# Optimization experiments

Measured on AMD Instinct MI355X. Metric: run time of the kernel, lower is better.

Reference implementation:

```python
import jax, jax.numpy as jnp
import numpy as np

B, M, L = 100, 100, 8
N = M * L
EPS = 1e-5  # torch BatchNorm2d default eps


def _conv(x, w, b, stride, pad):
    y = jax.lax.conv_general_dilated(x, w, (stride, stride), [(pad, pad), (pad, pad)],
                                     dimension_numbers=('NCHW', 'OIHW', 'NCHW'))
    return y + b[None, :, None, None]


def _convT(x, w, b, stride, pad):
    # torch ConvTranspose2d weight layout: (in_ch, out_ch, kH, kW)
    k = w.shape[2]
    wt = jnp.flip(w, (2, 3)).transpose(1, 0, 2, 3)  # -> OIHW
    p = k - 1 - pad
    y = jax.lax.conv_general_dilated(x, wt, (1, 1), [(p, p), (p, p)],
                                     lhs_dilation=(stride, stride),
                                     dimension_numbers=('NCHW', 'OIHW', 'NCHW'))
    return y + b[None, :, None, None]


def _bn(x):
    # BatchNorm2d constructed fresh in forward: weight=1, bias=0, batch stats (biased var)
    mean = x.mean(axis=(0, 2, 3), keepdims=True)
    var = x.var(axis=(0, 2, 3), keepdims=True)
    return (x - mean) / jnp.sqrt(var + EPS)


def _leaky(x):
    return jnp.where(x >= 0, x, 0.01 * x)


def _forward(x, conv1_w, conv1_b, conv2_w, conv2_b, conv3_w, conv3_b, conv4_w, conv4_b,
             fc_w, fc_b, dec_w, dec_b, ct1_w, ct1_b, ct2_w, ct2_b, ct3_w, ct3_b,
             ct4_w, ct4_b, ct5_w, ct5_b):
    # ---- encoder ----
    h = _bn(_leaky(_conv(x, conv1_w, conv1_b, 2, 1)))   # (B,128,32,32)
    h = _bn(_leaky(_conv(h, conv2_w, conv2_b, 2, 1)))   # (B,256,16,16)
    h = _bn(_leaky(_conv(h, conv3_w, conv3_b, 2, 1)))   # (B,1024,8,8)
    h = _bn(_leaky(_conv(h, conv4_w, conv4_b, 2, 1)))   # (B,1024,4,4)
    eig = jax.nn.relu(h.reshape(B, -1) @ fc_w + fc_b)   # (B, 800)
    # ---- latent_sample (training branch) ----
    sig = eig.reshape(B, M, L)
    row = jnp.sqrt(float(M * L)) * jnp.fft.ifft2(sig)          # complex (B,M,L)
    # original builds C via numpy/scipy per-sample -> detached; circulant[i,j] = c[(i-j) % n]
    row_flat = jax.lax.stop_gradient(row.real.reshape(B, N))
    i = jnp.arange(N)
    idx = (i[:, None] - i[None, :]) % N                        # (N,N) circulant gather
    C = row_flat[:, idx]                                       # (B,N,N)
    # original: Sigma_batch_eps[:, i] = eigenvalue (noise zeta is dead code), via numpy -> detached
    Y = jnp.fft.fft2(jax.lax.stop_gradient(sig)).real          # (B,M,L)
    # ---- decoder ----
    d = (Y.reshape(B, N) @ dec_w + dec_b).reshape(B, 1024, 3, 3)
    d = _convT(d, ct1_w, ct1_b, 2, 1)   # (B,512,5,5)
    d = _convT(d, ct2_w, ct2_b, 2, 0)   # (B,256,11,11)
    d = _convT(d, ct3_w, ct3_b, 2, 0)   # (B,128,23,23)
    d = _convT(d, ct4_w, ct4_b, 2, 0)   # (B,64,47,47)
    d = _convT(d, ct5_w, ct5_b, 1, 0)   # (B,1,49,49)
    return d, C, eig


def setup_inputs():
    key = jax.random.key(0)
    ks = jax.random.split(key, 16)

    def wv(k, shape, fan_in):
        return (jax.random.normal(k, shape, jnp.float32) / np.sqrt(fan_in)).astype(jnp.float32)

    return {
        'x': jax.random.normal(ks[0], (B, 1, 64, 64), jnp.float32),
        'conv1_w': wv(ks[1], (128, 1, 3, 3), 9), 'conv1_b': jnp.zeros((128,), jnp.float32),
        'conv2_w': wv(ks[2], (256, 128, 3, 3), 128 * 9), 'conv2_b': jnp.zeros((256,), jnp.float32),
        'conv3_w': wv(ks[3], (1024, 256, 3, 3), 256 * 9), 'conv3_b': jnp.zeros((1024,), jnp.float32),
        'conv4_w': wv(ks[4], (1024, 1024, 3, 3), 1024 * 9), 'conv4_b': jnp.zeros((1024,), jnp.float32),
        'fc_w': wv(ks[5], (1024 * 16, N), 1024 * 16), 'fc_b': jnp.zeros((N,), jnp.float32),
        'dec_w': wv(ks[6], (N, 1024 * 9), N), 'dec_b': jnp.zeros((1024 * 9,), jnp.float32),
        'ct1_w': wv(ks[7], (1024, 512, 3, 3), 1024 * 9), 'ct1_b': jnp.zeros((512,), jnp.float32),
        'ct2_w': wv(ks[8], (512, 256, 3, 3), 512 * 9), 'ct2_b': jnp.zeros((256,), jnp.float32),
        'ct3_w': wv(ks[9], (256, 128, 3, 3), 256 * 9), 'ct3_b': jnp.zeros((128,), jnp.float32),
        'ct4_w': wv(ks[10], (128, 64, 3, 3), 128 * 9), 'ct4_b': jnp.zeros((64,), jnp.float32),
        'ct5_w': wv(ks[11], (64, 1, 3, 3), 64 * 9), 'ct5_b': jnp.zeros((1,), jnp.float32),
    }


def reference(x, conv1_w, conv1_b, conv2_w, conv2_b, conv3_w, conv3_b, conv4_w, conv4_b,
              fc_w, fc_b, dec_w, dec_b, ct1_w, ct1_b, ct2_w, ct2_b, ct3_w, ct3_b,
              ct4_w, ct4_b, ct5_w, ct5_b):
    return _forward(x, conv1_w, conv1_b, conv2_w, conv2_b, conv3_w, conv3_b, conv4_w, conv4_b,
                    fc_w, fc_b, dec_w, dec_b, ct1_w, ct1_b, ct2_w, ct2_b, ct3_w, ct3_b,
                    ct4_w, ct4_b, ct5_w, ct5_b)
```

## Files before the change

kernel.cpp:

```cpp
#include <hip/hip_runtime.h>
#include <math.h>

typedef __attribute__((ext_vector_type(8))) short bf16x8;
typedef __attribute__((ext_vector_type(4))) float f32x4;
typedef unsigned short u16;

__device__ __forceinline__ u16 f2bf(float f) {
    unsigned u = __builtin_bit_cast(unsigned, f);
    u += 0x7FFFu + ((u >> 16) & 1u);
    return (u16)(u >> 16);
}
__device__ __forceinline__ float bf2f(u16 h) {
    unsigned u = ((unsigned)h) << 16;
    return __builtin_bit_cast(float, u);
}

template<int MODE, int OUT, int BM, int BN, int SWIZ, bool STATS, bool PF>
__global__ __launch_bounds__(256, 3)
void gemm(const u16* __restrict__ Abf, const u16* __restrict__ Bw,
          const float* __restrict__ bias, void* __restrict__ outv,
          float* __restrict__ stat,
          int M, int N, int K, int lgC,
          int IH, int IW, int OH, int OW, int zchunk)
{
    constexpr int ANSEG = BM / 64, BNSEG = BN / 64;
    constexpr int RM = BM / 32, RN = BN / 32;
    __shared__ __align__(16) u16 As[4 * BM * 8];
    __shared__ __align__(16) u16 Bs[4 * BN * 8];
    const int t = threadIdx.x;
    const int lane = t & 63, wave = t >> 6;
    const int lm = lane & 15, quad = lane >> 4;
    const int wm = wave & 1, wn = wave >> 1;
    int mt, nt, z;
    if (SWIZ == 1) {
        int mtN = (M + BM - 1) / BM;
        int id = blockIdx.x;
        nt = id & 7; int j = id >> 3;
        mt = j % mtN; z = j / mtN;
    } else { mt = blockIdx.x; nt = blockIdx.y; z = blockIdx.z; }
    const int k0 = z * zchunk, kend = k0 + zchunk;

    const int arow = (ANSEG == 2) ? (t >> 1) : (t >> 2);
    const int akb  = (ANSEG == 2) ? (t & 1) * 16 : (t & 3) * 8;
    const int a_gm = mt * BM + arow;
    const bool a_in = a_gm < M;
    int oy = 0, ox = 0, bimg = 0;
    if (MODE == 1) {
        int ohw = OH * OW;
        int g = a_in ? a_gm : 0;
        bimg = g / ohw; int r = g - bimg * ohw;
        oy = r / OW; ox = r - (r / OW) * OW;
    }
    const int brow = (BNSEG == 2) ? (t >> 1) : (t >> 2);
    const int bkb  = (BNSEG == 2) ? (t & 1) * 16 : (t & 3) * 8;
    const int b_gn = nt * BN + brow;
    const bool b_in = b_gn < N;

    const int Cmask = (1 << lgC) - 1;
    int ic_s = 0, tap_s = 0;
    bool aok = a_in;
    const u16* aptr;
    if (MODE == 0) {
        aptr = Abf + (size_t)a_gm * K + k0 + akb;
    } else {
        int kk0 = k0 + akb;
        tap_s = kk0 >> lgC; ic_s = kk0 & Cmask;
        int ky = tap_s / 3, kx = tap_s - (tap_s / 3) * 3;
        int iy = oy * 2 - 1 + ky, ix = ox * 2 - 1 + kx;
        aok = a_in && (unsigned)iy < (unsigned)IH && (unsigned)ix < (unsigned)IW;
        aptr = Abf + ((((size_t)bimg * IH + iy) * IW + ix) << lgC);
    }
    const u16* bptr = Bw + (size_t)b_gn * K + k0 + bkb;

    auto ldA = [&](uint4 (&v)[ANSEG]) {
        #pragma unroll
        for (int s = 0; s < ANSEG; s++) {
            uint4 x4 = make_uint4(0, 0, 0, 0);
            if (MODE == 0) {
                if (aok) x4 = *(const uint4*)(aptr + s * 8);
            } else {
                if (aok) x4 = *(const uint4*)(aptr + ic_s + s * 8);
            }
            v[s] = x4;
        }
        if (MODE == 0) {
            aptr += 32;
        } else {
            ic_s += 32;
            if (ic_s > Cmask) {
                ic_s -= Cmask + 1;
                tap_s++;
                int ky = tap_s / 3, kx = tap_s - (tap_s / 3) * 3;
                int iy = oy * 2 - 1 + ky, ix = ox * 2 - 1 + kx;
                aok = a_in && (unsigned)iy < (unsigned)IH && (unsigned)ix < (unsigned)IW;
                aptr = Abf + ((((size_t)bimg * IH + iy) * IW + ix) << lgC);
            }
        }
    };
    auto ldB = [&](uint4 (&v)[BNSEG]) {
        #pragma unroll
        for (int s = 0; s < BNSEG; s++) {
            uint4 x4 = make_uint4(0, 0, 0, 0);
            if (b_in) x4 = *(const uint4*)(bptr + s * 8);
            v[s] = x4;
        }
        bptr += 32;
    };

    f32x4 acc[RM][RN];
    #pragma unroll
    for (int i = 0; i < RM; i++)
        #pragma unroll
        for (int j = 0; j < RN; j++) acc[i][j] = (f32x4){0.f, 0.f, 0.f, 0.f};

    uint4 va[ANSEG], vb[BNSEG];
    if (PF) { ldA(va); ldB(vb); }
    for (int kb = k0; kb < kend; kb += 32) {
        if (!PF) { ldA(va); ldB(vb); }
        #pragma unroll
        for (int s = 0; s < ANSEG; s++)
            *(uint4*)&As[(((akb >> 3) + s) * BM + arow) * 8] = va[s];
        #pragma unroll
        for (int s = 0; s < BNSEG; s++)
            *(uint4*)&Bs[(((bkb >> 3) + s) * BN + brow) * 8] = vb[s];
        __syncthreads();
        if (PF && kb + 32 < kend) { ldA(va); ldB(vb); }
        bf16x8 af[RM], bfr[RN];
        #pragma unroll
        for (int i = 0; i < RM; i++)
            af[i] = *(const bf16x8*)&As[(size_t)(quad * BM + wm * (BM / 2) + i * 16 + lm) * 8];
        #pragma unroll
        for (int j = 0; j < RN; j++)
            bfr[j] = *(const bf16x8*)&Bs[(size_t)(quad * BN + wn * (BN / 2) + j * 16 + lm) * 8];
        #pragma unroll
        for (int i = 0; i < RM; i++)
            #pragma unroll
            for (int j = 0; j < RN; j++)
                acc[i][j] = __builtin_amdgcn_mfma_f32_16x16x32_bf16(af[i], bfr[j], acc[i][j], 0, 0, 0);
        __syncthreads();
    }

    const int n_base = nt * BN + wn * (BN / 2);
    const int m_base = mt * BM + wm * (BM / 2);
    int nj[RN]; float bvj[RN];
    #pragma unroll
    for (int j = 0; j < RN; j++) {
        nj[j] = n_base + j * 16 + lm;
        bvj[j] = 0.f;
        if (nj[j] < N && OUT != 4) {
            if (OUT == 0 || OUT == 5) bvj[j] = bias[nj[j]];
            else if (z == 0) bvj[j] = bias[nj[j]];
        }
    }
    if constexpr (OUT == 4) {
        float* op = (float*)outv;
        #pragma unroll
        for (int i = 0; i < RM; i++)
            #pragma unroll
            for (int r = 0; r < 4; r++) {
                int m = m_base + i * 16 + quad * 4 + r;
                if (m >= M) continue;
                #pragma unroll
                for (int j = 0; j < RN; j++)
                    if (nj[j] < N) atomicAdd(&op[(size_t)m * N + nj[j]], acc[i][j][r]);
            }
    } else if constexpr (OUT == 5) {
        u16* op = (u16*)outv;
        #pragma unroll
        for (int j = 0; j < RN; j++) {
            if (nj[j] >= N) continue;
            int c = nj[j] / 9, hw = nj[j] - c * 9;
            #pragma unroll
            for (int i = 0; i < RM; i++)
                #pragma unroll
                for (int r = 0; r < 4; r++) {
                    int m = m_base + i * 16 + quad * 4 + r;
                    if (m >= M) continue;
                    op[((size_t)m * 9 + hw) * 1024 + c] = f2bf(acc[i][j][r] + bvj[j]);
                }
        }
    } else if constexpr (OUT == 0) {
        int ohw = OH * OW;
        float sj[RN], qj[RN];
        #pragma unroll
        for (int j = 0; j < RN; j++) { sj[j] = 0.f; qj[j] = 0.f; }
        #pragma unroll
        for (int i = 0; i < RM; i++) {
            int m0 = m_base + i * 16 + quad * 4;
            if (m0 >= M) continue;
            int b = m0 / ohw, pix = m0 - b * ohw;
            #pragma unroll
            for (int j = 0; j < RN; j++) {
                if (nj[j] >= N) continue;
                #pragma unroll
                for (int r = 0; r < 4; r++) {
                    float val = acc[i][j][r] + bvj[j];
                    ((u16*)outv)[((size_t)b * ohw + pix + r) * N + nj[j]] = f2bf(val);
                    if (STATS) {
                        float lv = val >= 0.f ? val : 0.01f * val;
                        sj[j] += lv; qj[j] += lv * lv;
                    }
                }
            }
        }
        if constexpr (STATS) {
            #pragma unroll
            for (int j = 0; j < RN; j++) {
                float s = sj[j], q = qj[j];
                s += __shfl_down(s, 32); q += __shfl_down(q, 32);
                s += __shfl_down(s, 16); q += __shfl_down(q, 16);
                if (quad == 0 && nj[j] < N) {
                    atomicAdd(&stat[nj[j]], s);
                    atomicAdd(&stat[N + nj[j]], q);
                }
            }
        }
    } else {
        int ohw = OH * OW;
        #pragma unroll
        for (int i = 0; i < RM; i++) {
            int m0 = m_base + i * 16 + quad * 4;
            if (m0 >= M) continue;
            int b = m0 / ohw, pix = m0 - b * ohw;
            #pragma unroll
            for (int j = 0; j < RN; j++) {
                if (nj[j] >= N) continue;
                #pragma unroll
                for (int r = 0; r < 4; r++)
                    atomicAdd(&((float*)outv)[((size_t)b * ohw + pix + r) * N + nj[j]],
                              acc[i][j][r] + bvj[j]);
            }
        }
    }
}

template<int BM>
__global__ __launch_bounds__(256, 3)
void gemm_ct(const u16* __restrict__ Abf, const u16* __restrict__ Wb,
             const float* __restrict__ bias, u16* __restrict__ out,
             int N, int lgC, int IH, int IW, int OH, int OW,
             int4 Kc, int4 Mc, int4 Hc, int4 Wc, int4 Oc, int4 Dy, int4 Dx)
{
    constexpr int ANSEG = BM / 64;
    constexpr int RM = BM / 32, RN = 2;
    const int c = blockIdx.z;
    const int Ks[4] = {Kc.x, Kc.y, Kc.z, Kc.w};
    const int Ms[4] = {Mc.x, Mc.y, Mc.z, Mc.w};
    const int Hs[4] = {Hc.x, Hc.y, Hc.z, Hc.w};
    const int Wsz[4]= {Wc.x, Wc.y, Wc.z, Wc.w};
    const int Os[4] = {Oc.x, Oc.y, Oc.z, Oc.w};
    const int Dys[4]= {Dy.x, Dy.y, Dy.z, Dy.w};
    const int Dxs[4]= {Dx.x, Dx.y, Dx.z, Dx.w};
    const int K = Ks[c], M = Ms[c], OHc = Hs[c], OWc = Wsz[c];
    const int dyp = Dys[c], dxp = Dxs[c];
    const int mt = blockIdx.x, nt = blockIdx.y;
    if (mt * BM >= M) return;
    const u16* Bw = Wb + Os[c];

    __shared__ __align__(16) u16 As[4 * BM * 8];
    __shared__ __align__(16) u16 Bs[4 * 64 * 8];
    const int t = threadIdx.x;
    const int lane = t & 63, wave = t >> 6;
    const int lm = lane & 15, quad = lane >> 4;
    const int wm = wave & 1, wn = wave >> 1;

    const int arow = (ANSEG == 2) ? (t >> 1) : (t >> 2);
    const int akb  = (ANSEG == 2) ? (t & 1) * 16 : (t & 3) * 8;
    const int a_gm = mt * BM + arow;
    const bool a_in = a_gm < M;
    const int ohwc = OHc * OWc;
    int g = a_in ? a_gm : 0;
    int bimg = g / ohwc; int rr = g - bimg * ohwc;
    int oy = rr / OWc, ox = rr - (rr / OWc) * OWc;

    const int brow = t >> 2;
    const int bkb  = (t & 3) * 8;
    const int b_gn = nt * 64 + brow;
    const bool b_in = b_gn < N;

    const int Cmask = (1 << lgC) - 1;
    int ic_s = akb & Cmask;
    int ti_s = 0;
    bool aok; const u16* aptr;
    {
        int sh = 8 * (ti_s & 3);
        int dy = (int)(signed char)((dyp >> sh) & 255);
        int dx = (int)(signed char)((dxp >> sh) & 255);
        int iy = oy + dy, ix = ox + dx;
        aok = a_in && (unsigned)iy < (unsigned)IH && (unsigned)ix < (unsigned)IW;
        aptr = Abf + ((((size_t)bimg * IH + iy) * IW + ix) << lgC);
    }
    const u16* bptr = Bw + (size_t)b_gn * K + bkb;

    auto ldA = [&](uint4 (&v)[ANSEG]) {
        #pragma unroll
        for (int s = 0; s < ANSEG; s++) {
            uint4 x4 = make_uint4(0, 0, 0, 0);
            if (aok) x4 = *(const uint4*)(aptr + ic_s + s * 8);
            v[s] = x4;
        }
        ic_s += 32;
        if (ic_s > Cmask) {
            ic_s -= Cmask + 1;
            ti_s++;
            int sh = 8 * (ti_s & 3);
            int dy = (int)(signed char)((dyp >> sh) & 255);
            int dx = (int)(signed char)((dxp >> sh) & 255);
            int iy = oy + dy, ix = ox + dx;
            aok = a_in && (unsigned)iy < (unsigned)IH && (unsigned)ix < (unsigned)IW;
            aptr = Abf + ((((size_t)bimg * IH + iy) * IW + ix) << lgC);
        }
    };
    auto ldB = [&](uint4& v) {
        uint4 x4 = make_uint4(0, 0, 0, 0);
        if (b_in) x4 = *(const uint4*)bptr;
        v = x4;
        bptr += 32;
    };

    f32x4 acc[RM][RN];
    #pragma unroll
    for (int i = 0; i < RM; i++)
        #pragma unroll
        for (int j = 0; j < RN; j++) acc[i][j] = (f32x4){0.f, 0.f, 0.f, 0.f};

    uint4 va[ANSEG]; uint4 vb;
    ldA(va); ldB(vb);
    for (int kb = 0; kb < K; kb += 32) {
        #pragma unroll
        for (int s = 0; s < ANSEG; s++)
            *(uint4*)&As[(((akb >> 3) + s) * BM + arow) * 8] = va[s];
        *(uint4*)&Bs[((bkb >> 3) * 64 + brow) * 8] = vb;
        __syncthreads();
        if (kb + 32 < K) { ldA(va); ldB(vb); }
        bf16x8 af[RM], bfr[RN];
        #pragma unroll
        for (int i = 0; i < RM; i++)
            af[i] = *(const bf16x8*)&As[(size_t)(quad * BM + wm * (BM / 2) + i * 16 + lm) * 8];
        #pragma unroll
        for (int j = 0; j < RN; j++)
            bfr[j] = *(const bf16x8*)&Bs[(size_t)(quad * 64 + wn * 32 + j * 16 + lm) * 8];
        #pragma unroll
        for (int i = 0; i < RM; i++)
            #pragma unroll
            for (int j = 0; j < RN; j++)
                acc[i][j] = __builtin_amdgcn_mfma_f32_16x16x32_bf16(af[i], bfr[j], acc[i][j], 0, 0, 0);
        __syncthreads();
    }

    const int n_base = nt * 64 + wn * 32;
    const int m_base = mt * BM + wm * (BM / 2);
    const int cy = c >> 1, cx = c & 1;
    const int OHW = OH * OW;
    int nj[RN]; float bvj[RN];
    #pragma unroll
    for (int j = 0; j < RN; j++) {
        nj[j] = n_base + j * 16 + lm;
        bvj[j] = (nj[j] < N) ? bias[nj[j]] : 0.f;
    }
    #pragma unroll
    for (int i = 0; i < RM; i++)
        #pragma unroll
        for (int r = 0; r < 4; r++) {
            int m = m_base + i * 16 + quad * 4 + r;
            if (m >= M) continue;
            int b = m / ohwc, r2 = m - b * ohwc;
            int oyc = r2 / OWc, oxc = r2 - (r2 / OWc) * OWc;
            size_t ad0 = ((size_t)b * OHW + (2 * oyc + cy) * OW + 2 * oxc + cx) * N;
            #pragma unroll
            for (int j = 0; j < RN; j++)
                if (nj[j] < N) out[ad0 + nj[j]] = f2bf(acc[i][j][r] + bvj[j]);
        }
}

__global__ __launch_bounds__(256)
void convw_prep(const float* __restrict__ src, u16* __restrict__ dst, int lgC, int total) {
    int idx = blockIdx.x * 256 + threadIdx.x;
    if (idx >= total) return;
    int K = 9 << lgC;
    int oc = idx / K, kk = idx - oc * K;
    int tap = kk >> lgC, ic = kk & ((1 << lgC) - 1);
    dst[idx] = f2bf(src[(((size_t)oc << lgC) + ic) * 9 + tap]);
}

__global__ __launch_bounds__(256)
void transpose_cvt(const float* __restrict__ in, u16* __restrict__ out, int R, int C) {
    __shared__ float tl[32][33];
    int c0 = blockIdx.x * 32, r0 = blockIdx.y * 32;
    int tx = threadIdx.x & 31, ty = threadIdx.x >> 5;
    #pragma unroll
    for (int l = 0; l < 4; l++)
        tl[ty + 8 * l][tx] = in[(size_t)(r0 + ty + 8 * l) * C + c0 + tx];
    __syncthreads();
    #pragma unroll
    for (int l = 0; l < 4; l++)
        out[(size_t)(c0 + ty + 8 * l) * R + r0 + tx] = f2bf(tl[tx][ty + 8 * l]);
}

__global__ __launch_bounds__(256)
void ctw_fused(const float* __restrict__ in, u16* __restrict__ outw,
               int CIN, int P, int4 Kc, int4 Oc) {
    __shared__ float tl[32][33];
    int c0 = blockIdx.x * 32, r0 = blockIdx.y * 32;
    int C = gridDim.x * 32;
    int tx = threadIdx.x & 31, ty = threadIdx.x >> 5;
    #pragma unroll
    for (int l = 0; l < 4; l++)
        tl[ty + 8 * l][tx] = in[(size_t)(r0 + ty + 8 * l) * C + c0 + tx];
    __syncthreads();
    const int Ks[4] = {Kc.x, Kc.y, Kc.z, Kc.w};
    const int Os[4] = {Oc.x, Oc.y, Oc.z, Oc.w};
    int ic = r0 + tx;
    #pragma unroll
    for (int l = 0; l < 4; l++) {
        int cc = c0 + ty + 8 * l;
        int oc = cc / 9, tap = cc - 9 * oc;
        int ky = tap / 3, kx = tap - 3 * (tap / 3);
        int cyc = (P + ky) & 1, cxc = (P + kx) & 1;
        int cls = cyc * 2 + cxc;
        int nkx = ((P ^ cxc) & 1) ? 1 : 2;
        int ti = (ky >> 1) * nkx + (kx >> 1);
        outw[Os[cls] + (size_t)oc * Ks[cls] + ti * CIN + ic] = f2bf(tl[tx][ty + 8 * l]);
    }
}

__global__ __launch_bounds__(256)
void fcw_prep(const float* __restrict__ in, u16* __restrict__ out) {
    __shared__ float tl[32][33];
    int n0 = blockIdx.x * 32, c0 = blockIdx.y * 32, hw = blockIdx.z;
    int tx = threadIdx.x & 31, ty = threadIdx.x >> 5;
    #pragma unroll
    for (int l = 0; l < 4; l++)
        tl[ty + 8 * l][tx] = in[((size_t)(c0 + ty + 8 * l) * 16 + hw) * 800 + n0 + tx];
    __syncthreads();
    #pragma unroll
    for (int l = 0; l < 4; l++)
        out[(size_t)(n0 + ty + 8 * l) * 16384 + hw * 1024 + c0 + tx] = f2bf(tl[tx][ty + 8 * l]);
}

__global__ __launch_bounds__(256)
void wt5_prep(const float* __restrict__ in, u16* __restrict__ out) {
    int idx = blockIdx.x * 256 + threadIdx.x;
    if (idx >= 576) return;
    int tap = idx >> 6, ic = idx & 63;
    out[idx] = f2bf(in[ic * 9 + tap]);
}

__global__ __launch_bounds__(256)
void conv1_nhwc(const float* __restrict__ x, const float* __restrict__ w,
                const float* __restrict__ bias, u16* __restrict__ out) {
    int idx = blockIdx.x * 256 + threadIdx.x;
    if (idx >= 100 * 1024 * 128) return;
    int oc = idx & 127;
    int pix = (idx >> 7) & 1023;
    int b = idx >> 17;
    int oy = pix >> 5, ox = pix & 31;
    int iy0 = oy * 2 - 1, ix0 = ox * 2 - 1;
    float acc = bias[oc];
    const float* ip = x + (size_t)b * 4096;
    const float* wp = w + oc * 9;
    #pragma unroll
    for (int ky = 0; ky < 3; ky++) {
        int iy = iy0 + ky;
        if ((unsigned)iy >= 64u) continue;
        #pragma unroll
        for (int kx = 0; kx < 3; kx++) {
            int ix = ix0 + kx;
            if ((unsigned)ix >= 64u) continue;
            acc = fmaf(ip[iy * 64 + ix], wp[ky * 3 + kx], acc);
        }
    }
    out[idx] = f2bf(acc);
}

__global__ __launch_bounds__(256)
void bnstat8(const u16* __restrict__ x, float* __restrict__ accum, int C, int total) {
    __shared__ float ls[2048];
    for (int i = threadIdx.x; i < 2 * C; i += 256) ls[i] = 0.f;
    __syncthreads();
    int base = (blockIdx.x * 256 + threadIdx.x) * 8;
    int stride = gridDim.x * 256 * 8;
    float s[8], q[8];
    #pragma unroll
    for (int r = 0; r < 8; r++) { s[r] = 0.f; q[r] = 0.f; }
    for (int i = base; i < total; i += stride) {
        uint4 v = *(const uint4*)(x + i);
        const unsigned* w = (const unsigned*)&v;
        #pragma unroll
        for (int h = 0; h < 4; h++) {
            float v0 = __builtin_bit_cast(float, w[h] << 16);
            float v1 = __builtin_bit_cast(float, w[h] & 0xFFFF0000u);
            v0 = v0 >= 0.f ? v0 : 0.01f * v0;
            v1 = v1 >= 0.f ? v1 : 0.01f * v1;
            s[2 * h] += v0;     q[2 * h] += v0 * v0;
            s[2 * h + 1] += v1; q[2 * h + 1] += v1 * v1;
        }
    }
    int c0 = base & (C - 1);
    #pragma unroll
    for (int r = 0; r < 8; r++) {
        atomicAdd(&ls[c0 + r], s[r]);
        atomicAdd(&ls[C + c0 + r], q[r]);
    }
    __syncthreads();
    for (int i = threadIdx.x; i < 2 * C; i += 256) atomicAdd(&accum[i], ls[i]);
}

__global__ __launch_bounds__(256)
void bnapply8(const u16* __restrict__ x, u16* __restrict__ out,
              const float* __restrict__ accum, int C, int total, float invcnt) {
    int i8 = (blockIdx.x * 256 + threadIdx.x) * 8;
    if (i8 >= total) return;
    int c0 = i8 & (C - 1);
    uint4 v = *(const uint4*)(x + i8);
    const unsigned* w = (const unsigned*)&v;
    uint4 o;
    unsigned* ow = (unsigned*)&o;
    #pragma unroll
    for (int h = 0; h < 4; h++) {
        float m0 = accum[c0 + 2 * h] * invcnt, m1 = accum[c0 + 2 * h + 1] * invcnt;
        float q0 = accum[C + c0 + 2 * h] * invcnt, q1 = accum[C + c0 + 2 * h + 1] * invcnt;
        float in0 = rsqrtf(q0 - m0 * m0 + 1e-5f);
        float in1 = rsqrtf(q1 - m1 * m1 + 1e-5f);
        float v0 = __builtin_bit_cast(float, w[h] << 16);
        float v1 = __builtin_bit_cast(float, w[h] & 0xFFFF0000u);
        v0 = v0 >= 0.f ? v0 : 0.01f * v0;
        v1 = v1 >= 0.f ? v1 : 0.01f * v1;
        unsigned r0 = f2bf((v0 - m0) * in0);
        unsigned r1 = f2bf((v1 - m1) * in1);
        ow[h] = r0 | (r1 << 16);
    }
    *(uint4*)(out + i8) = o;
}

__global__ __launch_bounds__(256)
void bnstat4f(const float* __restrict__ x, float* __restrict__ accum, int C, int total) {
    __shared__ float ls[2048];
    for (int i = threadIdx.x; i < 2 * C; i += 256) ls[i] = 0.f;
    __syncthreads();
    int base = (blockIdx.x * 256 + threadIdx.x) * 4;
    int stride = gridDim.x * 1024;
    float s[4] = {0, 0, 0, 0}, q[4] = {0, 0, 0, 0};
    for (int i = base; i < total; i += stride) {
        f32x4 v = *(const f32x4*)(x + i);
        #pragma unroll
        for (int r = 0; r < 4; r++) {
            float vv = v[r]; vv = vv >= 0.f ? vv : 0.01f * vv;
            s[r] += vv; q[r] += vv * vv;
        }
    }
    int c0 = base & (C - 1);
    #pragma unroll
    for (int r = 0; r < 4; r++) {
        atomicAdd(&ls[c0 + r], s[r]);
        atomicAdd(&ls[C + c0 + r], q[r]);
    }
    __syncthreads();
    for (int i = threadIdx.x; i < 2 * C; i += 256) atomicAdd(&accum[i], ls[i]);
}

__global__ __launch_bounds__(256)
void bnapply4f(const float* __restrict__ x, u16* __restrict__ out,
               const float* __restrict__ accum, int C, int total, float invcnt) {
    int i4 = (blockIdx.x * 256 + threadIdx.x) * 4;
    if (i4 >= total) return;
    int c0 = i4 & (C - 1);
    f32x4 v = *(const f32x4*)(x + i4);
    unsigned r4[4];
    #pragma unroll
    for (int r = 0; r < 4; r++) {
        float m = accum[c0 + r] * invcnt;
        float var = accum[C + c0 + r] * invcnt - m * m;
        float inv = rsqrtf(var + 1e-5f);
        float vv = v[r]; vv = vv >= 0.f ? vv : 0.01f * vv;
        r4[r] = f2bf((vv - m) * inv);
    }
    *(uint2*)(out + i4) = make_uint2(r4[0] | (r4[1] << 16), r4[2] | (r4[3] << 16));
}

__global__ __launch_bounds__(256)
void finalize_relu(const float* __restrict__ acc, const float* __restrict__ bias,
                   float* __restrict__ out) {
    int i = blockIdx.x * 256 + threadIdx.x;
    if (i >= 100 * 800) return;
    float v = acc[i] + bias[i % 800];
    out[i] = fmaxf(v, 0.f);
}

__global__ __launch_bounds__(256)
void dft_real(const float* __restrict__ eig, float* __restrict__ Yr, u16* __restrict__ Yrb) {
    __shared__ float se[800];
    __shared__ float ctab[800];
    int b = blockIdx.x;
    for (int i = threadIdx.x; i < 800; i += 256) {
        se[i] = eig[b * 800 + i];
        ctab[i] = cospif(i * 0.0025f);
    }
    __syncthreads();
    int o0 = blockIdx.y * 400;
    for (int oi = o0 + threadIdx.x; oi < o0 + 400; oi += 256) {
        int k1 = oi >> 3, k2 = oi & 7;
        int d1 = k1 * 8, d2 = k2 * 100;
        float acc0 = 0.f, acc1 = 0.f;
        int p1 = 0;
        for (int n1 = 0; n1 < 100; n1 += 2) {
            int p = p1;
            #pragma unroll
            for (int n2 = 0; n2 < 8; n2++) {
                acc0 = fmaf(se[n1 * 8 + n2], ctab[p], acc0);
                p += d2; if (p >= 800) p -= 800;
            }
            int pb = p1 + d1; if (pb >= 800) pb -= 800;
            int p2 = pb;
            #pragma unroll
            for (int n2 = 0; n2 < 8; n2++) {
                acc1 = fmaf(se[(n1 + 1) * 8 + n2], ctab[p2], acc1);
                p2 += d2; if (p2 >= 800) p2 -= 800;
            }
            p1 = pb + d1; if (p1 >= 800) p1 -= 800;
        }
        float acc = acc0 + acc1;
        Yr[b * 800 + oi] = acc;
        Yrb[b * 800 + oi] = f2bf(acc);
    }
}

__global__ __launch_bounds__(256)
void build_C4(const float* __restrict__ Yr, float* __restrict__ C) {
    int idx = blockIdx.x * 256 + threadIdx.x;
    if (idx >= 100 * 800 * 200) return;
    int j4 = (idx % 200) * 4; int tt = idx / 200;
    int i = tt % 800;         int b = tt / 800;
    const float* y = Yr + b * 800;
    f32x4 v;
    #pragma unroll
    for (int r = 0; r < 4; r++) {
        int k = i - (j4 + r);
        k += (k >> 31) & 800;
        v[r] = y[k] * 0.035355339059327376f;
    }
    ((f32x4*)C)[idx] = v;
}

__global__ __launch_bounds__(256)
void convT5(const u16* __restrict__ in, const u16* __restrict__ w,
            const float* __restrict__ bias, float* __restrict__ out) {
    int idx = blockIdx.x * 256 + threadIdx.x;
    if (idx >= 100 * 49 * 49) return;
    int ox = idx % 49; int t2 = idx / 49;
    int oy = t2 % 49;  int b = t2 / 49;
    float ac[8];
    #pragma unroll
    for (int r = 0; r < 8; r++) ac[r] = 0.f;
    for (int ky = 0; ky < 3; ky++) {
        int iy = oy - ky;
        if ((unsigned)iy >= 47u) continue;
        for (int kx = 0; kx < 3; kx++) {
            int ix = ox - kx;
            if ((unsigned)ix >= 47u) continue;
            const uint4* ip = (const uint4*)(in + (((size_t)b * 47 + iy) * 47 + ix) * 64);
            const uint4* wp = (const uint4*)(w + (ky * 3 + kx) * 64);
            #pragma unroll
            for (int g = 0; g < 8; g++) {
                uint4 av = ip[g], wv = wp[g];
                const unsigned* aa = (const unsigned*)&av;
                const unsigned* ww = (const unsigned*)&wv;
                #pragma unroll
                for (int h = 0; h < 4; h++) {
                    float a0 = __builtin_bit_cast(float, aa[h] << 16);
                    float a1 = __builtin_bit_cast(float, aa[h] & 0xFFFF0000u);
                    float w0 = __builtin_bit_cast(float, ww[h] << 16);
                    float w1 = __builtin_bit_cast(float, ww[h] & 0xFFFF0000u);
                    int rix = ((g & 1) << 2) | h;
                    ac[rix] = fmaf(a0, w0, ac[rix]);
                    ac[rix] = fmaf(a1, w1, ac[rix]);
                }
            }
        }
    }
    out[idx] = bias[0] + ((ac[0] + ac[1]) + (ac[2] + ac[3]))
                       + ((ac[4] + ac[5]) + (ac[6] + ac[7]));
}

struct CTClass { int T, OHc, OWc, dyp, dxp, off, K; };
static void ct_params(int P, int OH, int OW, int CIN, int OC, CTClass cls[4]) {
    int off = 0;
    for (int c = 0; c < 4; c++) {
        int cy = c >> 1, cx = c & 1;
        int kys[2], dys[2], nky = 0, kxs[2], dxs[2], nkx = 0;
        for (int ky = 0; ky < 3; ky++)
            if (((cy + P + ky) & 1) == 0) { kys[nky] = ky; dys[nky] = (cy + P - ky) / 2; nky++; }
        for (int kx = 0; kx < 3; kx++)
            if (((cx + P + kx) & 1) == 0) { kxs[nkx] = kx; dxs[nkx] = (cx + P - kx) / 2; nkx++; }
        CTClass& cc = cls[c];
        cc.T = nky * nkx;
        cc.OHc = (OH - cy + 1) >> 1; cc.OWc = (OW - cx + 1) >> 1;
        cc.dyp = 0; cc.dxp = 0;
        int ti = 0;
        for (int a = 0; a < nky; a++)
            for (int b2 = 0; b2 < nkx; b2++, ti++) {
                cc.dyp |= (dys[a] & 255) << (8 * ti);
                cc.dxp |= (dxs[b2] & 255) << (8 * ti);
            }
        cc.off = off; cc.K = CIN * cc.T;
        off += OC * cc.K;
    }
}

template<int BM>
static void launch_ct(hipStream_t s, const u16* in, const u16* W, const float* bias, u16* outp,
                      int lgC, int OC, int IH, int IW, int OH, int OW, const CTClass* cls) {
    int maxMT = 0;
    for (int c = 0; c < 4; c++) {
        int mt = (100 * cls[c].OHc * cls[c].OWc + BM - 1) / BM;
        if (mt > maxMT) maxMT = mt;
    }
    dim3 g(maxMT, (OC + 63) / 64, 4);
    gemm_ct<BM><<<g, 256, 0, s>>>(in, W, bias, outp, OC, lgC, IH, IW, OH, OW,
        make_int4(cls[0].K, cls[1].K, cls[2].K, cls[3].K),
        make_int4(100*cls[0].OHc*cls[0].OWc, 100*cls[1].OHc*cls[1].OWc,
                  100*cls[2].OHc*cls[2].OWc, 100*cls[3].OHc*cls[3].OWc),
        make_int4(cls[0].OHc, cls[1].OHc, cls[2].OHc, cls[3].OHc),
        make_int4(cls[0].OWc, cls[1].OWc, cls[2].OWc, cls[3].OWc),
        make_int4(cls[0].off, cls[1].off, cls[2].off, cls[3].off),
        make_int4(cls[0].dyp, cls[1].dyp, cls[2].dyp, cls[3].dyp),
        make_int4(cls[0].dxp, cls[1].dxp, cls[2].dxp, cls[3].dxp));
}

static void launch_ctw(hipStream_t s, const float* w, u16* outw,
                       int CIN, int OC, int P, const CTClass* cls) {
    dim3 g((OC * 9) / 32, CIN / 32);
    ctw_fused<<<g, 256, 0, s>>>(w, outw, CIN, P,
        make_int4(cls[0].K, cls[1].K, cls[2].K, cls[3].K),
        make_int4(cls[0].off, cls[1].off, cls[2].off, cls[3].off));
}

extern "C" void kernel_launch(void* const* d_in, const int* in_sizes, int n_in,
                              void* d_out, int out_size, void* d_ws, size_t ws_size,
                              hipStream_t stream) {
    const float* x    = (const float*)d_in[0];
    const float* c1w  = (const float*)d_in[1];  const float* c1b = (const float*)d_in[2];
    const float* c2w  = (const float*)d_in[3];  const float* c2b = (const float*)d_in[4];
    const float* c3w  = (const float*)d_in[5];  const float* c3b = (const float*)d_in[6];
    const float* c4w  = (const float*)d_in[7];  const float* c4b = (const float*)d_in[8];
    const float* fcw  = (const float*)d_in[9];  const float* fcb = (const float*)d_in[10];
    const float* decw = (const float*)d_in[11]; const float* decb = (const float*)d_in[12];
    const float* t1w  = (const float*)d_in[13]; const float* t1b = (const float*)d_in[14];
    const float* t2w  = (const float*)d_in[15]; const float* t2b = (const float*)d_in[16];
    const float* t3w  = (const float*)d_in[17]; const float* t3b = (const float*)d_in[18];
    const float* t4w  = (const float*)d_in[19]; const float* t4b = (const float*)d_in[20];
    const float* t5w  = (const float*)d_in[21]; const float* t5b = (const float*)d_in[22];

    float* out = (float*)d_out;
    float* d_final = out;
    float* Cmat    = out + 240100;
    float* eig     = out + 240100 + 64000000;

    float* ws = (float*)d_ws;
    u16*   h1    = (u16*)(ws);
    u16*   W_fc  = (u16*)(ws);
    u16*   h2    = (u16*)(ws + 6553600);
    u16*   h3    = (u16*)(ws + 9830400);
    u16*   W_c2  = (u16*)(ws + 13107200);
    u16*   W_c3  = (u16*)(ws + 13254656);
    u16*   W_c4  = (u16*)(ws + 14434304);
    float* h4f   = ws + 19152896;
    u16*   h4    = (u16*)(ws + 20791296);
    float* accs  = ws + 21610496;
    float* facc  = ws + 21618688;
    float* Yr    = ws + 21698688;
    u16*   Yrb   = (u16*)(ws + 21778688);
    u16*   d0    = (u16*)(ws + 21818688);
    u16*   W_dec = (u16*)(ws + 22279488);
    float* acc1 = accs, *acc2 = accs + 2048, *acc3 = accs + 4096, *acc4 = accs + 6144;
    u16*   W_t   = (u16*)(ws);
    u16*   o1    = (u16*)(ws + 4718592);
    u16*   o2    = (u16*)(ws + 5358592);
    u16*   o3    = (u16*)(ws + 6907392);
    u16*   o4    = (u16*)(ws + 10292992);
    u16*   W_t5  = (u16*)(ws + 17361792);

    #define GRID(n) dim3(((n) + 255) / 256)

    hipMemsetAsync(accs, 0, (8192 + 80000) * 4, stream);

    conv1_nhwc<<<GRID(13107200), 256, 0, stream>>>(x, c1w, c1b, h1);
    bnstat8<<<1024, 256, 0, stream>>>(h1, acc1, 128, 13107200);
    bnapply8<<<GRID(1638400), 256, 0, stream>>>(h1, h1, acc1, 128, 13107200, 1.f / 102400.f);

    convw_prep<<<GRID(294912), 256, 0, stream>>>(c2w, W_c2, 7, 294912);
    gemm<1, 0, 128, 128, 0, true, false><<<dim3(200, 2, 1), 256, 0, stream>>>(
        h1, W_c2, c2b, h2, acc2, 25600, 256, 1152, 7, 32, 32, 16, 16, 1152);
    bnapply8<<<GRID(819200), 256, 0, stream>>>(h2, h2, acc2, 256, 6553600, 1.f / 25600.f);

    convw_prep<<<GRID(2359296), 256, 0, stream>>>(c3w, W_c3, 8, 2359296);
    gemm<1, 0, 128, 128, 1, true, false><<<dim3(400, 1, 1), 256, 0, stream>>>(
        h2, W_c3, c3b, h3, acc3, 6400, 1024, 2304, 8, 16, 16, 8, 8, 2304);
    bnapply8<<<GRID(819200), 256, 0, stream>>>(h3, h3, acc3, 1024, 6553600, 1.f / 6400.f);

    convw_prep<<<GRID(9437184), 256, 0, stream>>>(c4w, W_c4, 10, 9437184);
    hipMemsetAsync(h4f, 0, 1638400 * 4, stream);
    gemm<1, 1, 64, 128, 1, false, true><<<dim3(400, 1, 1), 256, 0, stream>>>(
        h3, W_c4, c4b, h4f, nullptr, 1600, 1024, 9216, 10, 8, 8, 4, 4, 4608);
    bnstat4f<<<1024, 256, 0, stream>>>(h4f, acc4, 1024, 1638400);
    bnapply4f<<<GRID(409600), 256, 0, stream>>>(h4f, h4, acc4, 1024, 1638400, 1.f / 1600.f);

    fcw_prep<<<dim3(25, 32, 16), 256, 0, stream>>>(fcw, W_fc);
    gemm<0, 4, 64, 64, 0, false, true><<<dim3(2, 13, 16), 256, 0, stream>>>(
        h4, W_fc, nullptr, facc, nullptr, 100, 800, 16384, 0, 0, 0, 0, 0, 1024);
    finalize_relu<<<GRID(80000), 256, 0, stream>>>(facc, fcb, eig);

    dft_real<<<dim3(100, 2), 256, 0, stream>>>(eig, Yr, Yrb);
    build_C4<<<GRID(16000000), 256, 0, stream>>>(Yr, Cmat);

    transpose_cvt<<<dim3(288, 25), 256, 0, stream>>>(decw, W_dec, 800, 9216);
    gemm<0, 5, 64, 64, 0, false, true><<<dim3(2, 144, 1), 256, 0, stream>>>(
        Yrb, W_dec, decb, d0, nullptr, 100, 9216, 800, 0, 0, 0, 0, 0, 800);

    CTClass c1c[4], c2c[4], c3c[4], c4c[4];
    ct_params(1, 5, 5, 1024, 512, c1c);
    ct_params(0, 11, 11, 512, 256, c2c);
    ct_params(0, 23, 23, 256, 128, c3c);
    ct_params(0, 47, 47, 128, 64, c4c);

    launch_ctw(stream, t1w, W_t, 1024, 512, 1, c1c);
    launch_ct<64>(stream, d0, W_t, t1b, o1, 10, 512, 3, 3, 5, 5, c1c);

    launch_ctw(stream, t2w, W_t, 512, 256, 0, c2c);
    launch_ct<64>(stream, o1, W_t, t2b, o2, 9, 256, 5, 5, 11, 11, c2c);

    launch_ctw(stream, t3w, W_t, 256, 128, 0, c3c);
    launch_ct<64>(stream, o2, W_t, t3b, o3, 8, 128, 11, 11, 23, 23, c3c);

    launch_ctw(stream, t4w, W_t, 128, 64, 0, c4c);
    launch_ct<128>(stream, o3, W_t, t4b, o4, 7, 64, 23, 23, 47, 47, c4c);

    wt5_prep<<<GRID(576), 256, 0, stream>>>(t5w, W_t5);
    convT5<<<GRID(240100), 256, 0, stream>>>(o4, W_t5, t5b, d_final);

    #undef GRID
}
```

Measured before the change: 1.134 ms.

## Fuse conv1 with BN stats, tile weight prep, permute dec weights, fuse relu

Conv1 now computes leaky-ReLU batch statistics as it writes its output, so the separate bnstat8 pass over the 26 MB activation is gone. convw_prep stages each output channel's weights in shared memory so the reordering reads are coalesced. The decoder weight transpose now permutes columns into (hw, c) order, which lets the dec GEMM write coalesced rows instead of scattered stores. finalize_relu is folded into dft_real, and conv2/conv3 GEMMs enable the PF template flag. The risks are fewer threads doing conv1 plus shared-memory atomics, and a shared-memory reduction that relies on blockDim matching 2×128 channels.

Measured after the change: 1.077 ms, median of 2. 1.05x faster.

```diff
diff --git a/kernel.cpp b/kernel.cpp
--- a/kernel.cpp
+++ b/kernel.cpp
@@ -148,7 +148,8 @@
         nj[j] = n_base + j * 16 + lm;
         bvj[j] = 0.f;
         if (nj[j] < N && OUT != 4) {
-            if (OUT == 0 || OUT == 5) bvj[j] = bias[nj[j]];
+            if (OUT == 0) bvj[j] = bias[nj[j]];
+            else if (OUT == 6) bvj[j] = bias[(nj[j] & 1023) * 9 + (nj[j] >> 10)];
             else if (z == 0) bvj[j] = bias[nj[j]];
         }
     }
@@ -164,21 +165,18 @@
                 for (int j = 0; j < RN; j++)
                     if (nj[j] < N) atomicAdd(&op[(size_t)m * N + nj[j]], acc[i][j][r]);
             }
-    } else if constexpr (OUT == 5) {
+    } else if constexpr (OUT == 6) {
         u16* op = (u16*)outv;
         #pragma unroll
-        for (int j = 0; j < RN; j++) {
-            if (nj[j] >= N) continue;
-            int c = nj[j] / 9, hw = nj[j] - c * 9;
-            #pragma unroll
-            for (int i = 0; i < RM; i++)
+        for (int i = 0; i < RM; i++)
+            #pragma unroll
+            for (int r = 0; r < 4; r++) {
+                int m = m_base + i * 16 + quad * 4 + r;
+                if (m >= M) continue;
                 #pragma unroll
-                for (int r = 0; r < 4; r++) {
-                    int m = m_base + i * 16 + quad * 4 + r;
-                    if (m >= M) continue;
-                    op[((size_t)m * 9 + hw) * 1024 + c] = f2bf(acc[i][j][r] + bvj[j]);
-                }
-        }
+                for (int j = 0; j < RN; j++)
+                    if (nj[j] < N) op[(size_t)m * N + nj[j]] = f2bf(acc[i][j][r] + bvj[j]);
+            }
     } else if constexpr (OUT == 0) {
         int ohw = OH * OW;
         float sj[RN], qj[RN];
@@ -374,27 +372,34 @@
 }
 
 __global__ __launch_bounds__(256)
-void convw_prep(const float* __restrict__ src, u16* __restrict__ dst, int lgC, int total) {
-    int idx = blockIdx.x * 256 + threadIdx.x;
-    if (idx >= total) return;
-    int K = 9 << lgC;
-    int oc = idx / K, kk = idx - oc * K;
-    int tap = kk >> lgC, ic = kk & ((1 << lgC) - 1);
-    dst[idx] = f2bf(src[(((size_t)oc << lgC) + ic) * 9 + tap]);
-}
-
-__global__ __launch_bounds__(256)
-void transpose_cvt(const float* __restrict__ in, u16* __restrict__ out, int R, int C) {
+void convw_prep(const float* __restrict__ src, u16* __restrict__ dst, int lgC) {
+    __shared__ float tl[9216];
+    int CIN = 1 << lgC;
+    int n = CIN * 9;
+    size_t base = (size_t)blockIdx.x * n;
+    for (int i = threadIdx.x; i < n; i += 256) tl[i] = src[base + i];
+    __syncthreads();
+    for (int j = threadIdx.x; j < n; j += 256) {
+        int tap = j >> lgC, ic = j & (CIN - 1);
+        dst[base + j] = f2bf(tl[ic * 9 + tap]);
+    }
+}
+
+__global__ __launch_bounds__(256)
+void transpose_cvt_dec(const float* __restrict__ in, u16* __restrict__ out) {
     __shared__ float tl[32][33];
     int c0 = blockIdx.x * 32, r0 = blockIdx.y * 32;
     int tx = threadIdx.x & 31, ty = threadIdx.x >> 5;
     #pragma unroll
     for (int l = 0; l < 4; l++)
-        tl[ty + 8 * l][tx] = in[(size_t)(r0 + ty + 8 * l) * C + c0 + tx];
+        tl[ty + 8 * l][tx] = in[(size_t)(r0 + ty + 8 * l) * 9216 + c0 + tx];
     __syncthreads();
     #pragma unroll
-    for (int l = 0; l < 4; l++)
-        out[(size_t)(c0 + ty + 8 * l) * R + r0 + tx] = f2bf(tl[tx][ty + 8 * l]);
+    for (int l = 0; l < 4; l++) {
+        int n = c0 + ty + 8 * l;
+        int cc = n / 9, hw = n - 9 * cc;
+        out[(size_t)(hw * 1024 + cc) * 800 + r0 + tx] = f2bf(tl[tx][ty + 8 * l]);
+    }
 }
 
 __global__ __launch_bounds__(256)
@@ -447,63 +452,46 @@
 }
 
 __global__ __launch_bounds__(256)
-void conv1_nhwc(const float* __restrict__ x, const float* __restrict__ w,
-                const float* __restrict__ bias, u16* __restrict__ out) {
-    int idx = blockIdx.x * 256 + threadIdx.x;
-    if (idx >= 100 * 1024 * 128) return;
-    int oc = idx & 127;
-    int pix = (idx >> 7) & 1023;
-    int b = idx >> 17;
-    int oy = pix >> 5, ox = pix & 31;
-    int iy0 = oy * 2 - 1, ix0 = ox * 2 - 1;
-    float acc = bias[oc];
-    const float* ip = x + (size_t)b * 4096;
+void conv1_stat(const float* __restrict__ x, const float* __restrict__ w,
+                const float* __restrict__ bias, u16* __restrict__ out,
+                float* __restrict__ accum) {
+    __shared__ float ls[256];
+    ls[threadIdx.x] = 0.f;
+    __syncthreads();
+    int idx0 = blockIdx.x * 256 + threadIdx.x;
+    int oc = idx0 & 127;
+    float wreg[9];
     const float* wp = w + oc * 9;
     #pragma unroll
-    for (int ky = 0; ky < 3; ky++) {
-        int iy = iy0 + ky;
-        if ((unsigned)iy >= 64u) continue;
-        #pragma unroll
-        for (int kx = 0; kx < 3; kx++) {
-            int ix = ix0 + kx;
-            if ((unsigned)ix >= 64u) continue;
-            acc = fmaf(ip[iy * 64 + ix], wp[ky * 3 + kx], acc);
-        }
-    }
-    out[idx] = f2bf(acc);
-}
-
-__global__ __launch_bounds__(256)
-void bnstat8(const u16* __restrict__ x, float* __restrict__ accum, int C, int total) {
-    __shared__ float ls[2048];
-    for (int i = threadIdx.x; i < 2 * C; i += 256) ls[i] = 0.f;
+    for (int k = 0; k < 9; k++) wreg[k] = wp[k];
+    float bz = bias[oc];
+    float s = 0.f, q = 0.f;
+    for (int idx = idx0; idx < 13107200; idx += 262144) {
+        int pix = (idx >> 7) & 1023;
+        int b = idx >> 17;
+        int oy = pix >> 5, ox = pix & 31;
+        int iy0 = oy * 2 - 1, ix0 = ox * 2 - 1;
+        float acc = bz;
+        const float* ip = x + (size_t)b * 4096;
+        #pragma unroll
+        for (int ky = 0; ky < 3; ky++) {
+            int iy = iy0 + ky;
+            if ((unsigned)iy >= 64u) continue;
+            #pragma unroll
+            for (int kx = 0; kx < 3; kx++) {
+                int ix = ix0 + kx;
+                if ((unsigned)ix >= 64u) continue;
+                acc = fmaf(ip[iy * 64 + ix], wreg[ky * 3 + kx], acc);
+            }
+        }
+        out[idx] = f2bf(acc);
+        float lv = acc >= 0.f ? acc : 0.01f * acc;
+        s += lv; q += lv * lv;
+    }
+    atomicAdd(&ls[oc], s);
+    atomicAdd(&ls[128 + oc], q);
     __syncthreads();
-    int base = (blockIdx.x * 256 + threadIdx.x) * 8;
-    int stride = gridDim.x * 256 * 8;
-    float s[8], q[8];
-    #pragma unroll
-    for (int r = 0; r < 8; r++) { s[r] = 0.f; q[r] = 0.f; }
-    for (int i = base; i < total; i += stride) {
-        uint4 v = *(const uint4*)(x + i);
-        const unsigned* w = (const unsigned*)&v;
-        #pragma unroll
-        for (int h = 0; h < 4; h++) {
-            float v0 = __builtin_bit_cast(float, w[h] << 16);
-            float v1 = __builtin_bit_cast(float, w[h] & 0xFFFF0000u);
-            v0 = v0 >= 0.f ? v0 : 0.01f * v0;
-            v1 = v1 >= 0.f ? v1 : 0.01f * v1;
-            s[2 * h] += v0;     q[2 * h] += v0 * v0;
-            s[2 * h + 1] += v1; q[2 * h + 1] += v1 * v1;
-        }
-    }
-    int c0 = base & (C - 1);
-    #pragma unroll
-    for (int r = 0; r < 8; r++) {
-        atomicAdd(&ls[c0 + r], s[r]);
-        atomicAdd(&ls[C + c0 + r], q[r]);
-    }
-    __syncthreads();
-    for (int i = threadIdx.x; i < 2 * C; i += 256) atomicAdd(&accum[i], ls[i]);
+    atomicAdd(&accum[threadIdx.x], ls[threadIdx.x]);
 }
 
 __global__ __launch_bounds__(256)
@@ -579,21 +567,15 @@
 }
 
 __global__ __launch_bounds__(256)
-void finalize_relu(const float* __restrict__ acc, const float* __restrict__ bias,
-                   float* __restrict__ out) {
-    int i = blockIdx.x * 256 + threadIdx.x;
-    if (i >= 100 * 800) return;
-    float v = acc[i] + bias[i % 800];
-    out[i] = fmaxf(v, 0.f);
-}
-
-__global__ __launch_bounds__(256)
-void dft_real(const float* __restrict__ eig, float* __restrict__ Yr, u16* __restrict__ Yrb) {
+void dft_real(const float* __restrict__ facc, const float* __restrict__ fcb,
+              float* __restrict__ eig, float* __restrict__ Yr, u16* __restrict__ Yrb) {
     __shared__ float se[800];
     __shared__ float ctab[800];
     int b = blockIdx.x;
     for (int i = threadIdx.x; i < 800; i += 256) {
-        se[i] = eig[b * 800 + i];
+        float v = fmaxf(facc[b * 800 + i] + fcb[i], 0.f);
+        se[i] = v;
+        if (blockIdx.y == 0) eig[b * 800 + i] = v;
         ctab[i] = cospif(i * 0.0025f);
     }
     __syncthreads();
@@ -784,21 +766,20 @@
 
     hipMemsetAsync(accs, 0, (8192 + 80000) * 4, stream);
 
-    conv1_nhwc<<<GRID(13107200), 256, 0, stream>>>(x, c1w, c1b, h1);
-    bnstat8<<<1024, 256, 0, stream>>>(h1, acc1, 128, 13107200);
+    conv1_stat<<<dim3(1024), 256, 0, stream>>>(x, c1w, c1b, h1, acc1);
     bnapply8<<<GRID(1638400), 256, 0, stream>>>(h1, h1, acc1, 128, 13107200, 1.f / 102400.f);
 
-    convw_prep<<<GRID(294912), 256, 0, stream>>>(c2w, W_c2, 7, 294912);
-    gemm<1, 0, 128, 128, 0, true, false><<<dim3(200, 2, 1), 256, 0, stream>>>(
+    convw_prep<<<dim3(256), 256, 0, stream>>>(c2w, W_c2, 7);
+    gemm<1, 0, 128, 128, 0, true, true><<<dim3(200, 2, 1), 256, 0, stream>>>(
         h1, W_c2, c2b, h2, acc2, 25600, 256, 1152, 7, 32, 32, 16, 16, 1152);
     bnapply8<<<GRID(819200), 256, 0, stream>>>(h2, h2, acc2, 256, 6553600, 1.f / 25600.f);
 
-    convw_prep<<<GRID(2359296), 256, 0, stream>>>(c3w, W_c3, 8, 2359296);
-    gemm<1, 0, 128, 128, 1, true, false><<<dim3(400, 1, 1), 256, 0, stream>>>(
+    convw_prep<<<dim3(1024), 256, 0, stream>>>(c3w, W_c3, 8);
+    gemm<1, 0, 128, 128, 1, true, true><<<dim3(400, 1, 1), 256, 0, stream>>>(
         h2, W_c3, c3b, h3, acc3, 6400, 1024, 2304, 8, 16, 16, 8, 8, 2304);
     bnapply8<<<GRID(819200), 256, 0, stream>>>(h3, h3, acc3, 1024, 6553600, 1.f / 6400.f);
 
-    convw_prep<<<GRID(9437184), 256, 0, stream>>>(c4w, W_c4, 10, 9437184);
+    convw_prep<<<dim3(1024), 256, 0, stream>>>(c4w, W_c4, 10);
     hipMemsetAsync(h4f, 0, 1638400 * 4, stream);
     gemm<1, 1, 64, 128, 1, false, true><<<dim3(400, 1, 1), 256, 0, stream>>>(
         h3, W_c4, c4b, h4f, nullptr, 1600, 1024, 9216, 10, 8, 8, 4, 4, 4608);
@@ -808,13 +789,12 @@
     fcw_prep<<<dim3(25, 32, 16), 256, 0, stream>>>(fcw, W_fc);
     gemm<0, 4, 64, 64, 0, false, true><<<dim3(2, 13, 16), 256, 0, stream>>>(
         h4, W_fc, nullptr, facc, nullptr, 100, 800, 16384, 0, 0, 0, 0, 0, 1024);
-    finalize_relu<<<GRID(80000), 256, 0, stream>>>(facc, fcb, eig);
-
-    dft_real<<<dim3(100, 2), 256, 0, stream>>>(eig, Yr, Yrb);
+
+    dft_real<<<dim3(100, 2), 256, 0, stream>>>(facc, fcb, eig, Yr, Yrb);
     build_C4<<<GRID(16000000), 256, 0, stream>>>(Yr, Cmat);
 
-    transpose_cvt<<<dim3(288, 25), 256, 0, stream>>>(decw, W_dec, 800, 9216);
-    gemm<0, 5, 64, 64, 0, false, true><<<dim3(2, 144, 1), 256, 0, stream>>>(
+    transpose_cvt_dec<<<dim3(288, 25), 256, 0, stream>>>(decw, W_dec);
+    gemm<0, 6, 64, 64, 0, false, true><<<dim3(2, 144, 1), 256, 0, stream>>>(
         Yrb, W_dec, decb, d0, nullptr, 100, 9216, 800, 0, 0, 0, 0, 0, 800);
 
     CTClass c1c[4], c2c[4], c3c[4], c4c[4];
```
